# Optimization experiments

Hardware: AMD Instinct MI355X
Metric: run time of the kernel (lower is better)

Reference implementation:

```python
import jax, jax.numpy as jnp
import numpy as np

B, N, C = 32, 577, 768
H = 12
DH = C // H  # 64
SCALE = DH ** -0.5


def setup_inputs() -> dict:
    key = jax.random.key(0)
    ks = jax.random.split(key, 5)
    x = jax.random.normal(ks[0], (B, N, C), dtype=jnp.float32)
    # Linear params (torch convention: y = x @ W.T + b)
    qkv_w = jax.random.normal(ks[1], (3 * C, C), dtype=jnp.float32) * (C ** -0.5)
    qkv_b = jnp.zeros((3 * C,), dtype=jnp.float32)
    proj_w = jax.random.normal(ks[2], (C, C), dtype=jnp.float32) * (C ** -0.5)
    proj_b = jnp.zeros((C,), dtype=jnp.float32)
    return {"x": x, "qkv_w": qkv_w, "qkv_b": qkv_b, "proj_w": proj_w, "proj_b": proj_b}


def reference(x, qkv_w, qkv_b, proj_w, proj_b):
    b, n, c = x.shape
    qkv = x @ qkv_w.T + qkv_b                       # [B, N, 3C]
    qkv = qkv.reshape(b, n, 3, H, DH).transpose(2, 0, 3, 1, 4)  # [3, B, H, N, DH]
    q, k, v = qkv[0], qkv[1], qkv[2]
    q = q * SCALE
    attn = jnp.einsum('bhnd,bhmd->bhnm', q, k)      # [B, H, N, N]
    # sigmoid -> inverse-sigmoid straight-through rewrite (forward equals logit(sigmoid(attn)))
    sig = jax.nn.sigmoid(attn)
    inv_sig = jnp.log(sig / (1.0 - sig))
    attn_st = attn + jax.lax.stop_gradient(inv_sig - attn)
    p = jax.nn.softmax(attn_st, axis=-1)
    out = jnp.einsum('bhnm,bhmd->bhnd', p, v)       # [B, H, N, DH]
    out = out.transpose(0, 2, 1, 3).reshape(b, n, c)
    return out @ proj_w.T + proj_b
```

## Files before the change

### kernel.cpp

```cpp
#include <hip/hip_runtime.h>

typedef __bf16 bf16;
typedef __attribute__((ext_vector_type(4))) __bf16 bf16x4;
typedef __attribute__((ext_vector_type(8))) __bf16 bf16x8;
typedef __attribute__((ext_vector_type(4))) float f32x4;

#define MFMA_BF16(A_, B_, C_) __builtin_amdgcn_mfma_f32_16x16x32_bf16(A_, B_, C_, 0, 0, 0)

#define BB    32
#define SEQ   577
#define CH    768
#define NH    12
#define DHD   64
#define MROWS (BB * SEQ)
#define NQKV  2304
#define SEQP  584
#define QSCALE 0.1803368801111204f

#define NSTEP 24

__device__ __forceinline__ void async_ld16(const bf16* g, bf16* l) {
  __builtin_amdgcn_global_load_lds(
      (const __attribute__((address_space(1))) void*)g,
      (__attribute__((address_space(3))) void*)l, 16, 0, 0);
}

__global__ __launch_bounds__(256) void cvt_bf16(const float* __restrict__ src,
                                                bf16* __restrict__ dst, int n) {
  int idx = (blockIdx.x * 256 + threadIdx.x) * 4;
  if (idx >= n) return;
  float4 v = *(const float4*)(src + idx);
  bf16x4 o = {(bf16)v.x, (bf16)v.y, (bf16)v.z, (bf16)v.w};
  *(bf16x4*)(dst + idx) = o;
}

__global__ __launch_bounds__(256) void pad_v(bf16* __restrict__ vt) {
  int r = blockIdx.x * 256 + threadIdx.x;
  if (r < BB * NH * DHD) {
    bf16* p = vt + (size_t)r * SEQP + SEQ;
#pragma unroll
    for (int i = 0; i < 7; ++i) p[i] = (bf16)0.f;
  }
}

__global__ __launch_bounds__(256, 2)
void gemm_qkv(const bf16* __restrict__ A, const bf16* __restrict__ W,
              const float* __restrict__ bias,
              bf16* __restrict__ qrm, bf16* __restrict__ krm, bf16* __restrict__ vt) {
  __shared__ bf16 As[2][128 * 32];
  __shared__ bf16 Bs[2][128 * 32];
  const int tid = threadIdx.x, lane = tid & 63, wid = tid >> 6;
  const int quad = lane >> 4, r15 = lane & 15;
  const int m0 = blockIdx.y * 128, n0 = blockIdx.x * 128;
  const int waveM = wid & 1, waveN = wid >> 1;

  const bf16* aSrc[2];
  const bf16* bSrc[2];
  for (int c = 0; c < 2; ++c) {
    int q = wid * 128 + c * 64 + lane;
    int row = q >> 2;
    int sw = (row ^ (row >> 2)) & 3;
    int kc = (q & 3) ^ sw;
    aSrc[c] = A + (size_t)(m0 + row) * CH + kc * 8;
    bSrc[c] = W + (size_t)(n0 + row) * CH + kc * 8;
  }

  f32x4 acc[4][4];
#pragma unroll
  for (int i = 0; i < 4; ++i)
#pragma unroll
    for (int j = 0; j < 4; ++j) acc[i][j] = (f32x4){0.f, 0.f, 0.f, 0.f};

#define GSTAGE(K0, BUF)                                                   \
  {                                                                       \
    _Pragma("unroll") for (int c = 0; c < 2; ++c) {                       \
      async_ld16(aSrc[c] + (K0), &As[BUF][(wid * 128 + c * 64) * 8]);     \
      async_ld16(bSrc[c] + (K0), &Bs[BUF][(wid * 128 + c * 64) * 8]);     \
    }                                                                     \
  }

#define GCOMPUTE(BUF)                                                     \
  {                                                                       \
    bf16x8 af[4], bfr[4];                                                 \
    _Pragma("unroll") for (int s = 0; s < 4; ++s) {                       \
      int rowA = waveM * 64 + s * 16 + r15;                               \
      int ca = quad ^ ((rowA ^ (rowA >> 2)) & 3);                         \
      af[s] = *(const bf16x8*)(&As[BUF][rowA * 32 + ca * 8]);             \
      int rowB = waveN * 64 + s * 16 + r15;                               \
      int cb = quad ^ ((rowB ^ (rowB >> 2)) & 3);                         \
      bfr[s] = *(const bf16x8*)(&Bs[BUF][rowB * 32 + cb * 8]);            \
    }                                                                     \
    _Pragma("unroll") for (int sm = 0; sm < 4; ++sm)                      \
      _Pragma("unroll") for (int sn = 0; sn < 4; ++sn)                    \
        acc[sm][sn] = MFMA_BF16(af[sm], bfr[sn], acc[sm][sn]);            \
  }

  GSTAGE(0, 0);
  for (int k0 = 0; k0 < CH; k0 += 64) {
    __syncthreads();
    GSTAGE(k0 + 32, 1);
    GCOMPUTE(0);
    __syncthreads();
    if (k0 + 64 < CH) GSTAGE(k0 + 64, 0);
    GCOMPUTE(1);
  }

  int t = (n0 >= 1536) ? 2 : (n0 >= 768 ? 1 : 0);
#pragma unroll
  for (int sn = 0; sn < 4; ++sn) {
    int gn = n0 + waveN * 64 + sn * 16 + r15;
    float bv = bias[gn];
    int col = gn - t * CH;
    int h = col >> 6, d = col & 63;
#pragma unroll
    for (int sm = 0; sm < 4; ++sm) {
      int gmBase = m0 + waveM * 64 + sm * 16 + quad * 4;
#pragma unroll
      for (int r = 0; r < 4; ++r) {
        int gm = gmBase + r;
        if (gm < MROWS) {
          float v = acc[sm][sn][r] + bv;
          if (t == 0) {
            qrm[(size_t)gm * CH + col] = (bf16)(v * QSCALE);
          } else if (t == 1) {
            krm[(size_t)gm * CH + col] = (bf16)v;
          } else {
            int b_ = gm / SEQ;
            int n_ = gm - b_ * SEQ;
            vt[((size_t)(b_ * NH + h) * DHD + d) * SEQP + n_] = (bf16)v;
          }
        }
      }
    }
  }
}
#undef GSTAGE
#undef GCOMPUTE

__global__ __launch_bounds__(512, 2)
void gemm_proj(const bf16* __restrict__ A, const bf16* __restrict__ W,
               const float* __restrict__ bias, float* __restrict__ out) {
  __shared__ bf16 As[4][256 * 32];
  __shared__ bf16 Bs[4][256 * 32];
  const int tid = threadIdx.x, lane = tid & 63, wid = tid >> 6;
  const int quad = lane >> 4, r15 = lane & 15;

  const int nbx = (int)gridDim.x;
  const int nwg = nbx * (int)gridDim.y;
  int bid = (int)blockIdx.y * nbx + (int)blockIdx.x;
  int q8 = nwg >> 3, r8 = nwg & 7;
  int xcd = bid & 7, sub = bid >> 3;
  int wg = (xcd < r8 ? xcd * (q8 + 1) : r8 * (q8 + 1) + (xcd - r8) * q8) + sub;
  const int m0 = (wg / nbx) * 256, n0 = (wg % nbx) * 256;

  const int rm = (wid >> 2) * 128;
  const int rn = (wid & 3) * 64;

  int aOff[2], bOff[2];
#pragma unroll
  for (int i = 0; i < 2; ++i) {
    int slot = i * 512 + tid;
    int row = slot >> 2, pc2 = slot & 3;
    int gc2 = pc2 ^ ((row ^ (row >> 2)) & 3);
    aOff[i] = (m0 + row) * CH + gc2 * 8;
    bOff[i] = (n0 + row) * CH + gc2 * 8;
  }

  f32x4 acc[8][4];
#pragma unroll
  for (int i = 0; i < 8; ++i)
#pragma unroll
    for (int j = 0; j < 4; ++j) acc[i][j] = (f32x4){0.f, 0.f, 0.f, 0.f};

#define ISSUE2(S)                                                              \
  {                                                                            \
    const int kb_ = (S) * 32;                                                  \
    const int bf_ = (S) & 3;                                                   \
    _Pragma("unroll") for (int i = 0; i < 2; ++i) {                            \
      async_ld16(A + aOff[i] + kb_, &As[bf_][(i * 512 + tid) * 8]);            \
      async_ld16(W + bOff[i] + kb_, &Bs[bf_][(i * 512 + tid) * 8]);            \
    }                                                                          \
  }

#define COMPUTE2(BF)                                                           \
  {                                                                            \
    bf16x8 bfr[4], afr[8];                                                     \
    _Pragma("unroll") for (int sn = 0; sn < 4; ++sn) {                         \
      int fr = rn + sn * 16 + r15;                                             \
      int pc2 = quad ^ ((fr ^ (fr >> 2)) & 3);                                 \
      bfr[sn] = *(const bf16x8*)(&Bs[BF][fr * 32 + pc2 * 8]);                  \
    }                                                                          \
    _Pragma("unroll") for (int sm = 0; sm < 8; ++sm) {                         \
      int fr = rm + sm * 16 + r15;                                             \
      int pc2 = quad ^ ((fr ^ (fr >> 2)) & 3);                                 \
      afr[sm] = *(const bf16x8*)(&As[BF][fr * 32 + pc2 * 8]);                  \
    }                                                                          \
    _Pragma("unroll") for (int sm = 0; sm < 8; ++sm)                           \
      _Pragma("unroll") for (int sn = 0; sn < 4; ++sn)                         \
        acc[sm][sn] = MFMA_BF16(afr[sm], bfr[sn], acc[sm][sn]);                \
  }

  ISSUE2(0);
  ISSUE2(1);
  for (int s = 0; s < NSTEP; ++s) {
    if (s < NSTEP - 2) {
      ISSUE2(s + 2);
      asm volatile("s_waitcnt vmcnt(8)" ::: "memory");
    } else if (s == NSTEP - 2) {
      asm volatile("s_waitcnt vmcnt(4)" ::: "memory");
    } else {
      asm volatile("s_waitcnt vmcnt(0)" ::: "memory");
    }
    __builtin_amdgcn_s_barrier();
    asm volatile("" ::: "memory");
    COMPUTE2(s & 3);
  }

#pragma unroll
  for (int sn = 0; sn < 4; ++sn) {
    int gn = n0 + rn + sn * 16 + r15;
    float bv = bias[gn];
#pragma unroll
    for (int sm = 0; sm < 8; ++sm) {
      int gmBase = m0 + rm + sm * 16 + quad * 4;
#pragma unroll
      for (int r = 0; r < 4; ++r) {
        int gm = gmBase + r;
        if (gm < MROWS) out[(size_t)gm * CH + gn] = acc[sm][sn][r] + bv;
      }
    }
  }
}
#undef ISSUE2
#undef COMPUTE2

__global__ __launch_bounds__(256, 5)
void attn_kernel(const bf16* __restrict__ qrm, const bf16* __restrict__ krm,
                 const bf16* __restrict__ vt, bf16* __restrict__ ob) {
  __shared__ bf16 Ks[64 * 72];
  __shared__ bf16 Vt[64 * 72];
  __shared__ bf16 Ps[4][16 * 72];
  const int tid = threadIdx.x, lane = tid & 63, wid = tid >> 6;
  const int quad = lane >> 4, r15 = lane & 15;
  const int qt = blockIdx.x, bh = blockIdx.y;
  const int b_ = bh / NH, h = bh - b_ * NH;
  const bf16* vtb = vt + (size_t)bh * DHD * SEQP;

  bf16x8 qf[2][2];
#pragma unroll
  for (int g = 0; g < 2; ++g) {
    int qrow = qt * 128 + wid * 32 + g * 16 + r15;
    if (qrow > SEQ - 1) qrow = SEQ - 1;
    const bf16* qp = qrm + (size_t)(b_ * SEQ + qrow) * CH + h * DHD + quad * 8;
    qf[g][0] = *(const bf16x8*)qp;
    qf[g][1] = *(const bf16x8*)(qp + 32);
  }

  f32x4 oacc[2][4];
#pragma unroll
  for (int g = 0; g < 2; ++g)
#pragma unroll
    for (int i = 0; i < 4; ++i) oacc[g][i] = (f32x4){0.f, 0.f, 0.f, 0.f};
  float lrow[2][4] = {{0.f, 0.f, 0.f, 0.f}, {0.f, 0.f, 0.f, 0.f}};

  bf16* Pw = Ps[wid];

  for (int j0 = 0; j0 < SEQ; j0 += 64) {
    __syncthreads();
#pragma unroll
    for (int c = 0; c < 2; ++c) {
      int sid = c * 256 + tid;
      int row = sid >> 3, cc = sid & 7;
      int jr = j0 + row;
      if (jr > SEQ - 1) jr = SEQ - 1;
      *(bf16x8*)(Ks + row * 72 + cc * 8) =
          *(const bf16x8*)(krm + (size_t)(b_ * SEQ + jr) * CH + h * DHD + cc * 8);
      int jst = j0 + cc * 8;
      if (jst > SEQ - 1) jst = SEQ - 1;
      *(bf16x8*)(Vt + row * 72 + cc * 8) = *(const bf16x8*)(vtb + (size_t)row * SEQP + jst);
    }
    __syncthreads();

#pragma unroll
    for (int g = 0; g < 2; ++g) {
      f32x4 s[4];
#pragma unroll
      for (int sj = 0; sj < 4; ++sj) {
        bf16x8 kf0 = *(const bf16x8*)(Ks + (sj * 16 + r15) * 72 + quad * 8);
        bf16x8 kf1 = *(const bf16x8*)(Ks + (sj * 16 + r15) * 72 + 32 + quad * 8);
        f32x4 z = (f32x4){0.f, 0.f, 0.f, 0.f};
        s[sj] = MFMA_BF16(qf[g][0], kf0, z);
        s[sj] = MFMA_BF16(qf[g][1], kf1, s[sj]);
      }
#pragma unroll
      for (int sj = 0; sj < 4; ++sj)
        if (j0 + sj * 16 + r15 > SEQ - 1) s[sj] = (f32x4){-1e30f, -1e30f, -1e30f, -1e30f};

#pragma unroll
      for (int sj = 0; sj < 4; ++sj)
#pragma unroll
        for (int r = 0; r < 4; ++r) {
          float e = __builtin_amdgcn_exp2f(s[sj][r]);
          s[sj][r] = e;
          lrow[g][r] += e;
        }

#pragma unroll
      for (int sj = 0; sj < 4; ++sj)
#pragma unroll
        for (int r = 0; r < 4; ++r)
          Pw[(quad * 4 + r) * 72 + sj * 16 + r15] = (bf16)s[sj][r];
      asm volatile("s_waitcnt lgkmcnt(0)" ::: "memory");

#pragma unroll
      for (int kc = 0; kc < 2; ++kc) {
        bf16x8 pf = *(const bf16x8*)(Pw + r15 * 72 + kc * 32 + quad * 8);
#pragma unroll
        for (int sd = 0; sd < 4; ++sd) {
          bf16x8 vf = *(const bf16x8*)(Vt + (sd * 16 + r15) * 72 + kc * 32 + quad * 8);
          oacc[g][sd] = MFMA_BF16(pf, vf, oacc[g][sd]);
        }
      }
    }
  }

#pragma unroll
  for (int g = 0; g < 2; ++g)
#pragma unroll
    for (int r = 0; r < 4; ++r) {
      float rs = lrow[g][r];
      rs += __shfl_xor(rs, 1);
      rs += __shfl_xor(rs, 2);
      rs += __shfl_xor(rs, 4);
      rs += __shfl_xor(rs, 8);
      lrow[g][r] = rs;
    }

#pragma unroll
  for (int g = 0; g < 2; ++g)
#pragma unroll
    for (int r = 0; r < 4; ++r) {
      int orow = qt * 128 + wid * 32 + g * 16 + quad * 4 + r;
      if (orow < SEQ) {
        float inv = 1.0f / lrow[g][r];
        size_t rowoff = ((size_t)(b_ * SEQ + orow)) * CH + h * DHD;
#pragma unroll
        for (int sd = 0; sd < 4; ++sd)
          ob[rowoff + sd * 16 + r15] = (bf16)(oacc[g][sd][r] * inv);
      }
    }
}

extern "C" void kernel_launch(void* const* d_in, const int* in_sizes, int n_in,
                              void* d_out, int out_size, void* d_ws, size_t ws_size,
                              hipStream_t stream) {
  const float* x      = (const float*)d_in[0];
  const float* qkv_w  = (const float*)d_in[1];
  const float* qkv_b  = (const float*)d_in[2];
  const float* proj_w = (const float*)d_in[3];
  const float* proj_b = (const float*)d_in[4];
  float* out = (float*)d_out;

  char* w = (char*)d_ws;
  bf16* xb  = (bf16*)(w);
  bf16* wqp = (bf16*)(w + 28360704);
  bf16* qrm = (bf16*)(w + 31899648);
  bf16* krm = (bf16*)(w + 60260352);
  bf16* vtb = (bf16*)(w + 88621056);

  cvt_bf16<<<(MROWS * CH / 4 + 255) / 256, 256, 0, stream>>>(x, xb, MROWS * CH);
  cvt_bf16<<<(NQKV * CH / 4 + 255) / 256, 256, 0, stream>>>(qkv_w, wqp, NQKV * CH);
  pad_v<<<(BB * NH * DHD + 255) / 256, 256, 0, stream>>>(vtb);

  gemm_qkv<<<dim3(NQKV / 128, 145), 256, 0, stream>>>(
      xb, wqp, qkv_b, qrm, krm, vtb);

  attn_kernel<<<dim3(5, BB * NH), 256, 0, stream>>>(qrm, krm, vtb, xb);

  cvt_bf16<<<(CH * CH / 4 + 255) / 256, 256, 0, stream>>>(proj_w, wqp, CH * CH);

  gemm_proj<<<dim3(CH / 256, 73), 512, 0, stream>>>(xb, wqp, proj_b, out);
}
```

Before: 376.7 us.

## Transpose S=K·Q^T in attention so P stores vectorize and interleave both row groups

Swaps the MFMA operand order for the score computation so each lane holds consecutive key columns of one query row. P can then be written to LDS as bf16x4 vectors, and the row-sum reduction shrinks to two cross-quad shuffles. The two 16-row query groups are processed together, with separate P buffers, to interleave independent MFMAs. This costs more LDS and registers, so the occupancy hint is lowered from 5 to 4 blocks.

```diff
diff --git a/kernel.cpp b/kernel.cpp
--- a/kernel.cpp
+++ b/kernel.cpp
@@ -234,12 +234,12 @@
 #undef ISSUE2
 #undef COMPUTE2
 
-__global__ __launch_bounds__(256, 5)
+__global__ __launch_bounds__(256, 4)
 void attn_kernel(const bf16* __restrict__ qrm, const bf16* __restrict__ krm,
                  const bf16* __restrict__ vt, bf16* __restrict__ ob) {
   __shared__ bf16 Ks[64 * 72];
   __shared__ bf16 Vt[64 * 72];
-  __shared__ bf16 Ps[4][16 * 72];
+  __shared__ bf16 Ps[4][2][16 * 72];
   const int tid = threadIdx.x, lane = tid & 63, wid = tid >> 6;
   const int quad = lane >> 4, r15 = lane & 15;
   const int qt = blockIdx.x, bh = blockIdx.y;
@@ -261,9 +261,10 @@
   for (int g = 0; g < 2; ++g)
 #pragma unroll
     for (int i = 0; i < 4; ++i) oacc[g][i] = (f32x4){0.f, 0.f, 0.f, 0.f};
-  float lrow[2][4] = {{0.f, 0.f, 0.f, 0.f}, {0.f, 0.f, 0.f, 0.f}};
-
-  bf16* Pw = Ps[wid];
+  float lrow0 = 0.f, lrow1 = 0.f;
+
+  bf16* P0 = &Ps[wid][0][0];
+  bf16* P1 = &Ps[wid][1][0];
 
   for (int j0 = 0; j0 < SEQ; j0 += 64) {
     __syncthreads();
@@ -281,74 +282,73 @@
     }
     __syncthreads();
 
-#pragma unroll
-    for (int g = 0; g < 2; ++g) {
-      f32x4 s[4];
-#pragma unroll
-      for (int sj = 0; sj < 4; ++sj) {
-        bf16x8 kf0 = *(const bf16x8*)(Ks + (sj * 16 + r15) * 72 + quad * 8);
-        bf16x8 kf1 = *(const bf16x8*)(Ks + (sj * 16 + r15) * 72 + 32 + quad * 8);
-        f32x4 z = (f32x4){0.f, 0.f, 0.f, 0.f};
-        s[sj] = MFMA_BF16(qf[g][0], kf0, z);
-        s[sj] = MFMA_BF16(qf[g][1], kf1, s[sj]);
-      }
-#pragma unroll
-      for (int sj = 0; sj < 4; ++sj)
-        if (j0 + sj * 16 + r15 > SEQ - 1) s[sj] = (f32x4){-1e30f, -1e30f, -1e30f, -1e30f};
-
-#pragma unroll
-      for (int sj = 0; sj < 4; ++sj)
-#pragma unroll
-        for (int r = 0; r < 4; ++r) {
-          float e = __builtin_amdgcn_exp2f(s[sj][r]);
-          s[sj][r] = e;
-          lrow[g][r] += e;
-        }
-
-#pragma unroll
-      for (int sj = 0; sj < 4; ++sj)
-#pragma unroll
-        for (int r = 0; r < 4; ++r)
-          Pw[(quad * 4 + r) * 72 + sj * 16 + r15] = (bf16)s[sj][r];
-      asm volatile("s_waitcnt lgkmcnt(0)" ::: "memory");
-
-#pragma unroll
-      for (int kc = 0; kc < 2; ++kc) {
-        bf16x8 pf = *(const bf16x8*)(Pw + r15 * 72 + kc * 32 + quad * 8);
-#pragma unroll
-        for (int sd = 0; sd < 4; ++sd) {
-          bf16x8 vf = *(const bf16x8*)(Vt + (sd * 16 + r15) * 72 + kc * 32 + quad * 8);
-          oacc[g][sd] = MFMA_BF16(pf, vf, oacc[g][sd]);
-        }
-      }
-    }
-  }
-
-#pragma unroll
-  for (int g = 0; g < 2; ++g)
+    f32x4 s0[4], s1[4];
+#pragma unroll
+    for (int sj = 0; sj < 4; ++sj) {
+      bf16x8 kf0 = *(const bf16x8*)(Ks + (sj * 16 + r15) * 72 + quad * 8);
+      bf16x8 kf1 = *(const bf16x8*)(Ks + (sj * 16 + r15) * 72 + 32 + quad * 8);
+      f32x4 z = (f32x4){0.f, 0.f, 0.f, 0.f};
+      s0[sj] = MFMA_BF16(kf0, qf[0][0], z);
+      s0[sj] = MFMA_BF16(kf1, qf[0][1], s0[sj]);
+      s1[sj] = MFMA_BF16(kf0, qf[1][0], z);
+      s1[sj] = MFMA_BF16(kf1, qf[1][1], s1[sj]);
+    }
+
+#pragma unroll
+    for (int sj = 0; sj < 4; ++sj)
+#pragma unroll
+      for (int r = 0; r < 4; ++r) {
+        int j = j0 + sj * 16 + quad * 4 + r;
+        float e0 = (j <= SEQ - 1) ? __builtin_amdgcn_exp2f(s0[sj][r]) : 0.f;
+        float e1 = (j <= SEQ - 1) ? __builtin_amdgcn_exp2f(s1[sj][r]) : 0.f;
+        s0[sj][r] = e0; lrow0 += e0;
+        s1[sj][r] = e1; lrow1 += e1;
+      }
+
+#pragma unroll
+    for (int sj = 0; sj < 4; ++sj) {
+      bf16x4 p0 = {(bf16)s0[sj][0], (bf16)s0[sj][1], (bf16)s0[sj][2], (bf16)s0[sj][3]};
+      bf16x4 p1 = {(bf16)s1[sj][0], (bf16)s1[sj][1], (bf16)s1[sj][2], (bf16)s1[sj][3]};
+      *(bf16x4*)(P0 + r15 * 72 + sj * 16 + quad * 4) = p0;
+      *(bf16x4*)(P1 + r15 * 72 + sj * 16 + quad * 4) = p1;
+    }
+    asm volatile("s_waitcnt lgkmcnt(0)" ::: "memory");
+
+#pragma unroll
+    for (int kc = 0; kc < 2; ++kc) {
+      bf16x8 pf0 = *(const bf16x8*)(P0 + r15 * 72 + kc * 32 + quad * 8);
+      bf16x8 pf1 = *(const bf16x8*)(P1 + r15 * 72 + kc * 32 + quad * 8);
+#pragma unroll
+      for (int sd = 0; sd < 4; ++sd) {
+        bf16x8 vf = *(const bf16x8*)(Vt + (sd * 16 + r15) * 72 + kc * 32 + quad * 8);
+        oacc[0][sd] = MFMA_BF16(pf0, vf, oacc[0][sd]);
+        oacc[1][sd] = MFMA_BF16(pf1, vf, oacc[1][sd]);
+      }
+    }
+  }
+
+  lrow0 += __shfl_xor(lrow0, 16);
+  lrow0 += __shfl_xor(lrow0, 32);
+  lrow1 += __shfl_xor(lrow1, 16);
+  lrow1 += __shfl_xor(lrow1, 32);
+
+#pragma unroll
+  for (int g = 0; g < 2; ++g) {
+    float lr = (g == 0) ? lrow0 : lrow1;
 #pragma unroll
     for (int r = 0; r < 4; ++r) {
-      float rs = lrow[g][r];
-      rs += __shfl_xor(rs, 1);
-      rs += __shfl_xor(rs, 2);
-      rs += __shfl_xor(rs, 4);
-      rs += __shfl_xor(rs, 8);
-      lrow[g][r] = rs;
-    }
-
-#pragma unroll
-  for (int g = 0; g < 2; ++g)
-#pragma unroll
-    for (int r = 0; r < 4; ++r) {
-      int orow = qt * 128 + wid * 32 + g * 16 + quad * 4 + r;
+      int m = quad * 4 + r;
+      float rs = __shfl(lr, m);
+      int orow = qt * 128 + wid * 32 + g * 16 + m;
       if (orow < SEQ) {
-        float inv = 1.0f / lrow[g][r];
+        float inv = 1.0f / rs;
         size_t rowoff = ((size_t)(b_ * SEQ + orow)) * CH + h * DHD;
 #pragma unroll
         for (int sd = 0; sd < 4; ++sd)
           ob[rowoff + sd * 16 + r15] = (bf16)(oacc[g][sd][r] * inv);
       }
     }
+  }
 }
 
 extern "C" void kernel_launch(void* const* d_in, const int* in_sizes, int n_in,
```

Result: faster. 361.2 us (-4.1%).
